# Optimization experiments

Measured on AMD Instinct MI355X. Metric: run time of the kernel, lower is better.

## Reference

```python
import jax, jax.numpy as jnp
import numpy as np

L = 19                      # blur kernel side
K2 = L * L                  # 361 taps
PAD1 = L // 2               # 9 (left/top)
PAD2 = L // 2               # 9 (right/bottom, l odd)


def _sv_blur(x, kernel):
    """Spatially-varying blur: out[b,c,i,j] = sum_k patch_k(x)[b,c,i,j]*kernel[b,k,i,j] / K2.

    Divisor: the torch module always recomputes divisor = fold(unfold(ones)).sum(1)
    (padded size H+18 != 128 init size), and with fold kernel_size=1 this is the
    constant L*L everywhere.
    """
    B, C, H, W = x.shape
    pad = jnp.pad(x, ((0, 0), (0, 0), (PAD1, PAD2), (PAD1, PAD2)), mode='reflect')
    # Extract LxL patches per pixel; single-channel batch of B*C maps, so output
    # channel ordering is row-major over (u, v) kernel offsets, matching torch unfold.
    xr = pad.reshape(B * C, 1, H + PAD1 + PAD2, W + PAD1 + PAD2)
    patches = jax.lax.conv_general_dilated_patches(
        xr, filter_shape=(L, L), window_strides=(1, 1), padding='VALID')  # [B*C, K2, H, W]
    patches = patches.reshape(B, C, K2, H, W)
    out = jnp.einsum('bckhw,bkhw->bchw', patches, kernel)
    return out / jnp.asarray(K2, dtype=out.dtype)


def setup_inputs() -> dict:
    key = jax.random.key(0)
    k1, k2 = jax.random.split(key)
    B, C, H, W = 2, 3, 256, 256
    inp = jax.random.normal(k1, (B, C, H, W), dtype=jnp.float32)
    kernel = jax.random.uniform(k2, (B, K2, H, W), dtype=jnp.float32)
    return {"input": inp, "kernel": kernel}


def reference(input, kernel):
    return _sv_blur(input, kernel)
```

## Files before the change

### kernel.cpp

```cpp
#include <hip/hip_runtime.h>


#define LW     19
#define PAD    9
#define K2     361
#define HH     256
#define WW     256
#define CC     3
#define HW     (HH * WW)
#define TPX    2
#define TX     64
#define TY     4
#define TILE_W (TX * TPX)
#define TILE_H TY
#define SM_W   (TILE_W + LW - 1)
#define SM_H   (TILE_H + LW - 1)

#define PREFETCH_ROW(u_, buf_)                                              \
  {                                                                         \
    _Pragma("unroll")                                                       \
    for (int v = 0; v < LW; ++v)                                            \
      (buf_)[v] = *(const float2*)(kp + (size_t)((u_) * LW + v) * HW);      \
  }

#define COMPUTE_ROW(u_, buf_)                                               \
  {                                                                         \
    _Pragma("unroll")                                                       \
    for (int c = 0; c < CC; ++c) {                                          \
      const float* wp = &tile[c][ty + (u_)][tx * TPX];                      \
      float2 w[10];                                                         \
      _Pragma("unroll")                                                     \
      for (int q = 0; q < 10; ++q) w[q] = *(const float2*)(wp + q * 2);     \
      _Pragma("unroll")                                                     \
      for (int v = 0; v < LW; ++v) {                                        \
        const float xe = ((v) & 1) ? w[(v) >> 1].y : w[(v) >> 1].x;         \
        const float xo = (((v) + 1) & 1) ? w[((v) + 1) >> 1].y              \
                                         : w[((v) + 1) >> 1].x;             \
        acc[c].x = fmaf(xe, (buf_)[v].x, acc[c].x);                         \
        acc[c].y = fmaf(xo, (buf_)[v].y, acc[c].y);                         \
      }                                                                     \
    }                                                                       \
  }

__global__ __launch_bounds__(256)
void svblur_kernel(const float* __restrict__ x,
                   const float* __restrict__ ker,
                   float* __restrict__ out) {
    __shared__ float tile[CC][SM_H][SM_W];

    const int tx  = threadIdx.x;
    const int ty  = threadIdx.y;
    const int tid = ty * TX + tx;
    const int j0  = blockIdx.x * TILE_W;
    const int i0  = blockIdx.y * TILE_H;
    const int b   = blockIdx.z;

    const int i  = i0 + ty;
    const int jj = j0 + tx * TPX;
    const float* kp = ker + ((size_t)b * K2 * HH + i) * WW + jj;

    float2 bufA[LW], bufB[LW];
    PREFETCH_ROW(0, bufA);

    const float* xb = x + (size_t)b * CC * HW;
    for (int idx = tid; idx < CC * SM_H * SM_W; idx += TX * TY) {
        int c  = idx / (SM_H * SM_W);
        int rm = idx - c * (SM_H * SM_W);
        int r  = rm / SM_W;
        int cc = rm - r * SM_W;
        int gr = i0 + r - PAD;
        gr = gr < 0 ? -gr : (gr >= HH ? 2 * HH - 2 - gr : gr);
        int gc = j0 + cc - PAD;
        gc = gc < 0 ? -gc : (gc >= WW ? 2 * WW - 2 - gc : gc);
        ((float*)tile)[idx] = xb[((size_t)c * HH + gr) * WW + gc];
    }
    __syncthreads();

    float2 acc[CC] = {};

    #pragma unroll
    for (int u = 0; u < LW - 1; u += 2) {
        PREFETCH_ROW(u + 1, bufB);
        COMPUTE_ROW(u, bufA);
        PREFETCH_ROW(u + 2, bufA);
        COMPUTE_ROW(u + 1, bufB);
    }
    COMPUTE_ROW(LW - 1, bufA);

    const float s = 1.0f / (float)K2;
    float* op = out + (((size_t)b * CC) * HH + i) * WW + jj;
    #pragma unroll
    for (int c = 0; c < CC; ++c) {
        float2 r;
        r.x = acc[c].x * s;
        r.y = acc[c].y * s;
        *(float2*)(op + (size_t)c * HW) = r;
    }
}

extern "C" void kernel_launch(void* const* d_in, const int* in_sizes, int n_in,
                              void* d_out, int out_size, void* d_ws, size_t ws_size,
                              hipStream_t stream) {
    const float* x   = (const float*)d_in[0];
    const float* ker = (const float*)d_in[1];
    float* out       = (float*)d_out;

    dim3 grid(WW / TILE_W, HH / TILE_H, 2);
    dim3 block(TX, TY, 1);
    svblur_kernel<<<grid, block, 0, stream>>>(x, ker, out);
}
```

Baseline: 264.7 us.

## Split kernel-row reduction across four blocks and add partial-sum reduce kernel

The 19 kernel rows are now split into four chunks of five (four for the last), each handled by a separate block along grid z, which gives four times as many blocks. Each block writes partial sums to workspace, and a second kernel adds the four partials and scales the result. This is meant to raise occupancy and memory-level parallelism on a grid that had only 256 blocks. The cost is an extra launch, extra partial traffic through workspace, and more redundant halo loads per block.

```diff
diff --git a/kernel.cpp b/kernel.cpp
--- a/kernel.cpp
+++ b/kernel.cpp
@@ -14,20 +14,23 @@
 #define TILE_W (TX * TPX)
 #define TILE_H TY
 #define SM_W   (TILE_W + LW - 1)
-#define SM_H   (TILE_H + LW - 1)
+#define NSPLIT 4
+#define NU_MAX 5
+#define SM_H   (TILE_H + NU_MAX - 1)
 
-#define PREFETCH_ROW(u_, buf_)                                              \
+#define PREFETCH_ROW(du_, buf_)                                             \
   {                                                                         \
+    const float* kq = kp + (size_t)((du_) * LW) * HW;                       \
     _Pragma("unroll")                                                       \
     for (int v = 0; v < LW; ++v)                                            \
-      (buf_)[v] = *(const float2*)(kp + (size_t)((u_) * LW + v) * HW);      \
+      (buf_)[v] = *(const float2*)(kq + (size_t)v * HW);                    \
   }
 
-#define COMPUTE_ROW(u_, buf_)                                               \
+#define COMPUTE_ROW(du_, buf_)                                              \
   {                                                                         \
     _Pragma("unroll")                                                       \
     for (int c = 0; c < CC; ++c) {                                          \
-      const float* wp = &tile[c][ty + (u_)][tx * TPX];                      \
+      const float* wp = &tile[c][ty + (du_)][tx * TPX];                     \
       float2 w[10];                                                         \
       _Pragma("unroll")                                                     \
       for (int q = 0; q < 10; ++q) w[q] = *(const float2*)(wp + q * 2);     \
@@ -43,9 +46,9 @@
   }
 
 __global__ __launch_bounds__(256)
-void svblur_kernel(const float* __restrict__ x,
-                   const float* __restrict__ ker,
-                   float* __restrict__ out) {
+void svblur_part(const float* __restrict__ x,
+                 const float* __restrict__ ker,
+                 float* __restrict__ part) {
     __shared__ float tile[CC][SM_H][SM_W];
 
     const int tx  = threadIdx.x;
@@ -53,11 +56,15 @@
     const int tid = ty * TX + tx;
     const int j0  = blockIdx.x * TILE_W;
     const int i0  = blockIdx.y * TILE_H;
-    const int b   = blockIdx.z;
+    const int zz  = blockIdx.z;
+    const int b   = zz >> 2;
+    const int s   = zz & 3;
+    const int u0  = s * NU_MAX;
+    const int nuM1 = (s == 3) ? 3 : 4;
 
     const int i  = i0 + ty;
     const int jj = j0 + tx * TPX;
-    const float* kp = ker + ((size_t)b * K2 * HH + i) * WW + jj;
+    const float* kp = ker + (((size_t)b * K2 + u0 * LW) * HH + i) * WW + jj;
 
     float2 bufA[LW], bufB[LW];
     PREFETCH_ROW(0, bufA);
@@ -68,7 +75,7 @@
         int rm = idx - c * (SM_H * SM_W);
         int r  = rm / SM_W;
         int cc = rm - r * SM_W;
-        int gr = i0 + r - PAD;
+        int gr = i0 + u0 + r - PAD;
         gr = gr < 0 ? -gr : (gr >= HH ? 2 * HH - 2 - gr : gr);
         int gc = j0 + cc - PAD;
         gc = gc < 0 ? -gc : (gc >= WW ? 2 * WW - 2 - gc : gc);
@@ -78,24 +85,40 @@
 
     float2 acc[CC] = {};
 
+    PREFETCH_ROW(1, bufB);
+    COMPUTE_ROW(0, bufA);
+    PREFETCH_ROW(2, bufA);
+    COMPUTE_ROW(1, bufB);
+    PREFETCH_ROW(3, bufB);
+    COMPUTE_ROW(2, bufA);
+    PREFETCH_ROW(((4 < nuM1 ? 4 : nuM1)), bufA);
+    COMPUTE_ROW(3, bufB);
+    if (nuM1 == 4) { COMPUTE_ROW(4, bufA); }
+
+    float* pp = part + ((size_t)zz * CC) * HW + (size_t)i * WW + jj;
     #pragma unroll
-    for (int u = 0; u < LW - 1; u += 2) {
-        PREFETCH_ROW(u + 1, bufB);
-        COMPUTE_ROW(u, bufA);
-        PREFETCH_ROW(u + 2, bufA);
-        COMPUTE_ROW(u + 1, bufB);
-    }
-    COMPUTE_ROW(LW - 1, bufA);
+    for (int c = 0; c < CC; ++c)
+        *(float2*)(pp + (size_t)c * HW) = acc[c];
+}
 
-    const float s = 1.0f / (float)K2;
-    float* op = out + (((size_t)b * CC) * HH + i) * WW + jj;
-    #pragma unroll
-    for (int c = 0; c < CC; ++c) {
-        float2 r;
-        r.x = acc[c].x * s;
-        r.y = acc[c].y * s;
-        *(float2*)(op + (size_t)c * HW) = r;
-    }
+__global__ __launch_bounds__(256)
+void svblur_reduce(const float* __restrict__ part, float* __restrict__ out) {
+    const int PLANE4 = CC * HW / 4;
+    const int gid = blockIdx.x * 256 + threadIdx.x;
+    const int b = gid / PLANE4;
+    const int within = gid - b * PLANE4;
+    const float4* p4 = (const float4*)part;
+    float4 s0 = p4[(size_t)(b * NSPLIT + 0) * PLANE4 + within];
+    float4 s1 = p4[(size_t)(b * NSPLIT + 1) * PLANE4 + within];
+    float4 s2 = p4[(size_t)(b * NSPLIT + 2) * PLANE4 + within];
+    float4 s3 = p4[(size_t)(b * NSPLIT + 3) * PLANE4 + within];
+    const float sc = 1.0f / (float)K2;
+    float4 r;
+    r.x = (s0.x + s1.x + s2.x + s3.x) * sc;
+    r.y = (s0.y + s1.y + s2.y + s3.y) * sc;
+    r.z = (s0.z + s1.z + s2.z + s3.z) * sc;
+    r.w = (s0.w + s1.w + s2.w + s3.w) * sc;
+    ((float4*)out)[gid] = r;
 }
 
 extern "C" void kernel_launch(void* const* d_in, const int* in_sizes, int n_in,
@@ -104,8 +127,13 @@
     const float* x   = (const float*)d_in[0];
     const float* ker = (const float*)d_in[1];
     float* out       = (float*)d_out;
+    float* part      = (float*)d_ws;
 
-    dim3 grid(WW / TILE_W, HH / TILE_H, 2);
-    dim3 block(TX, TY, 1);
-    svblur_kernel<<<grid, block, 0, stream>>>(x, ker, out);
+    dim3 g1(WW / TILE_W, HH / TILE_H, 2 * NSPLIT);
+    dim3 b1(TX, TY, 1);
+    svblur_part<<<g1, b1, 0, stream>>>(x, ker, part);
+
+    dim3 g2((2 * CC * HW / 4) / 256, 1, 1);
+    dim3 b2(256, 1, 1);
+    svblur_reduce<<<g2, b2, 0, stream>>>(part, out);
 }
```

New measurement: 264.3 us. About the same (-0.2%).
